# Kernel optimization log

Measured on AMD Instinct MI355X. Metric: run time of the kernel, lower is better.

## Reference

```python
import jax, jax.numpy as jnp
import numpy as np

N_NEURON = 128
N_RULES = 512
BATCH = 4096


def setup_inputs() -> dict:
    key = jax.random.key(0)
    k1, k2, k3, k4, k5 = jax.random.split(key, 5)
    x = jax.random.normal(k1, (N_NEURON, BATCH, N_RULES), dtype=jnp.float32)
    head_w = jax.random.normal(k2, (N_NEURON, N_RULES), dtype=jnp.float32) * (1.0 / np.sqrt(N_RULES))
    head_b = jax.random.normal(k3, (N_NEURON,), dtype=jnp.float32) * 0.01
    foot_w = jax.random.normal(k4, (2, N_NEURON), dtype=jnp.float32) * (1.0 / np.sqrt(N_NEURON))
    foot_b = jax.random.normal(k5, (2,), dtype=jnp.float32) * 0.01
    return {"x": x, "head_w": head_w, "head_b": head_b, "foot_w": foot_w, "foot_b": foot_b}


def reference(x, head_w, head_b, foot_w, foot_b):
    # Fused form of the per-neuron Linear(n_rules, 1) loop:
    # head[b, n] = x[n, b, :] @ head_w[n, :] + head_b[n]
    head = jnp.einsum("nbr,nr->bn", x, head_w) + head_b  # [B, n_neuron]
    logits = head @ foot_w.T + foot_b                      # [B, 2]
    return jax.nn.softmax(logits, axis=-1)
```

## Files before the change

### kernel.cpp

```cpp
#include <hip/hip_runtime.h>

#define BATCH   4096
#define NRULES  512
#define NNEUR   128

typedef float f32x4 __attribute__((ext_vector_type(4)));

__global__ __launch_bounds__(256) void head_kernel(
    const float* __restrict__ x,
    const float* __restrict__ head_w,
    const float* __restrict__ head_b,
    float* __restrict__ head_t)
{
    const int lane = threadIdx.x & 63;
    const int wave = threadIdx.x >> 6;
    const long long wave_g = (long long)blockIdx.x * 4 + wave;
    const long long rid0 = wave_g * 8;
    const int n  = (int)(rid0 >> 12);
    const int b0 = (int)(rid0 & (BATCH - 1));

    const f32x4* w4 = (const f32x4*)(head_w + (size_t)n * NRULES);
    const f32x4 wA = w4[lane];
    const f32x4 wB = w4[64 + lane];

    const float* xrow = x + rid0 * NRULES;
    float acc[8];
#pragma unroll
    for (int j = 0; j < 8; ++j) {
        const f32x4* xr = (const f32x4*)(xrow + (size_t)j * NRULES);
        f32x4 a = __builtin_nontemporal_load(xr + lane);
        f32x4 b = __builtin_nontemporal_load(xr + 64 + lane);
        acc[j] = a[0]*wA[0] + a[1]*wA[1] + a[2]*wA[2] + a[3]*wA[3]
               + b[0]*wB[0] + b[1]*wB[1] + b[2]*wB[2] + b[3]*wB[3];
    }

#pragma unroll
    for (int j = 0; j < 8; ++j) {
#pragma unroll
        for (int off = 32; off > 0; off >>= 1)
            acc[j] += __shfl_xor(acc[j], off, 64);
    }

    if (lane < 8) {
        float v = (lane == 0) ? acc[0]
                : (lane == 1) ? acc[1]
                : (lane == 2) ? acc[2]
                : (lane == 3) ? acc[3]
                : (lane == 4) ? acc[4]
                : (lane == 5) ? acc[5]
                : (lane == 6) ? acc[6]
                              : acc[7];
        v += head_b[n];
        head_t[(size_t)n * BATCH + b0 + lane] = v;
    }
}

__global__ __launch_bounds__(64) void foot_kernel(
    const float* __restrict__ head_t,
    const float* __restrict__ foot_w,
    const float* __restrict__ foot_b,
    float* __restrict__ out)
{
    const int b = blockIdx.x * 64 + threadIdx.x;

    float l0 = foot_b[0];
    float l1 = foot_b[1];
#pragma unroll 16
    for (int n = 0; n < NNEUR; ++n) {
        const float h = head_t[(size_t)n * BATCH + b];
        l0 = fmaf(h, foot_w[n], l0);
        l1 = fmaf(h, foot_w[NNEUR + n], l1);
    }

    const float m  = fmaxf(l0, l1);
    const float e0 = __expf(l0 - m);
    const float e1 = __expf(l1 - m);
    const float inv = 1.0f / (e0 + e1);
    float2 r;
    r.x = e0 * inv;
    r.y = e1 * inv;
    *(float2*)(out + 2 * b) = r;
}

extern "C" void kernel_launch(void* const* d_in, const int* in_sizes, int n_in,
                              void* d_out, int out_size, void* d_ws, size_t ws_size,
                              hipStream_t stream) {
    const float* x      = (const float*)d_in[0];
    const float* head_w = (const float*)d_in[1];
    const float* head_b = (const float*)d_in[2];
    const float* foot_w = (const float*)d_in[3];
    const float* foot_b = (const float*)d_in[4];
    float* out    = (float*)d_out;
    float* head_t = (float*)d_ws;

    const int grid1 = (NNEUR * BATCH) / (8 * 4);
    head_kernel<<<grid1, 256, 0, stream>>>(x, head_w, head_b, head_t);

    foot_kernel<<<BATCH / 64, 64, 0, stream>>>(head_t, foot_w, foot_b, out);
}
```

Before: 1.257 ms.

## Restructure head kernel to 8 rows per wave-pass and split foot reduction

```diff
diff --git a/kernel.cpp b/kernel.cpp
--- a/kernel.cpp
+++ b/kernel.cpp
@@ -13,73 +13,82 @@
     float* __restrict__ head_t)
 {
     const int lane = threadIdx.x & 63;
-    const int wave = threadIdx.x >> 6;
-    const long long wave_g = (long long)blockIdx.x * 4 + wave;
-    const long long rid0 = wave_g * 8;
-    const int n  = (int)(rid0 >> 12);
-    const int b0 = (int)(rid0 & (BATCH - 1));
+    const int wv   = threadIdx.x >> 6;
+    const int i    = lane & 7;
+    const int q    = lane >> 3;
 
-    const f32x4* w4 = (const f32x4*)(head_w + (size_t)n * NRULES);
-    const f32x4 wA = w4[lane];
-    const f32x4 wB = w4[64 + lane];
+    const int wg    = blockIdx.x * 4 + wv;
+    const int n     = wg >> 6;
+    const int bbase = (wg & 63) << 6;
 
-    const float* xrow = x + rid0 * NRULES;
-    float acc[8];
+    const f32x4* wp = (const f32x4*)(head_w + (size_t)n * NRULES);
+    f32x4 w[16];
 #pragma unroll
-    for (int j = 0; j < 8; ++j) {
-        const f32x4* xr = (const f32x4*)(xrow + (size_t)j * NRULES);
-        f32x4 a = __builtin_nontemporal_load(xr + lane);
-        f32x4 b = __builtin_nontemporal_load(xr + 64 + lane);
-        acc[j] = a[0]*wA[0] + a[1]*wA[1] + a[2]*wA[2] + a[3]*wA[3]
-               + b[0]*wB[0] + b[1]*wB[1] + b[2]*wB[2] + b[3]*wB[3];
-    }
+    for (int k = 0; k < 16; ++k) w[k] = wp[i + 8 * k];
 
+    const float hb = head_b[n];
+    float* hrow = head_t + (size_t)n * BATCH;
+
+#pragma unroll 1
+    for (int c = 0; c < 8; ++c) {
+        const int b0 = bbase + c * 8;
+        const f32x4* xp =
+            (const f32x4*)(x + ((size_t)n * BATCH + b0 + q) * NRULES);
+        f32x4 acc = {0.0f, 0.0f, 0.0f, 0.0f};
 #pragma unroll
-    for (int j = 0; j < 8; ++j) {
-#pragma unroll
-        for (int off = 32; off > 0; off >>= 1)
-            acc[j] += __shfl_xor(acc[j], off, 64);
-    }
-
-    if (lane < 8) {
-        float v = (lane == 0) ? acc[0]
-                : (lane == 1) ? acc[1]
-                : (lane == 2) ? acc[2]
-                : (lane == 3) ? acc[3]
-                : (lane == 4) ? acc[4]
-                : (lane == 5) ? acc[5]
-                : (lane == 6) ? acc[6]
-                              : acc[7];
-        v += head_b[n];
-        head_t[(size_t)n * BATCH + b0 + lane] = v;
+        for (int k = 0; k < 16; ++k) {
+            f32x4 v = xp[i + 8 * k];
+            acc += v * w[k];
+        }
+        float s = (acc[0] + acc[1]) + (acc[2] + acc[3]);
+        s += __shfl_xor(s, 1, 64);
+        s += __shfl_xor(s, 2, 64);
+        s += __shfl_xor(s, 4, 64);
+        if (i == 0) hrow[b0 + q] = s + hb;
     }
 }
 
-__global__ __launch_bounds__(64) void foot_kernel(
+__global__ __launch_bounds__(512) void foot_kernel(
     const float* __restrict__ head_t,
     const float* __restrict__ foot_w,
     const float* __restrict__ foot_b,
     float* __restrict__ out)
 {
-    const int b = blockIdx.x * 64 + threadIdx.x;
+    __shared__ float p0[4][128];
+    __shared__ float p1[4][128];
 
-    float l0 = foot_b[0];
-    float l1 = foot_b[1];
-#pragma unroll 16
-    for (int n = 0; n < NNEUR; ++n) {
-        const float h = head_t[(size_t)n * BATCH + b];
+    const int t  = threadIdx.x;
+    const int bl = t & 127;
+    const int qt = t >> 7;
+    const int b0 = blockIdx.x * 128;
+
+    float l0 = 0.0f, l1 = 0.0f;
+    const int n0 = qt * 32;
+#pragma unroll 8
+    for (int k = 0; k < 32; ++k) {
+        const int n = n0 + k;
+        const float h = head_t[(size_t)n * BATCH + b0 + bl];
         l0 = fmaf(h, foot_w[n], l0);
         l1 = fmaf(h, foot_w[NNEUR + n], l1);
     }
+    p0[qt][bl] = l0;
+    p1[qt][bl] = l1;
+    __syncthreads();
 
-    const float m  = fmaxf(l0, l1);
-    const float e0 = __expf(l0 - m);
-    const float e1 = __expf(l1 - m);
-    const float inv = 1.0f / (e0 + e1);
-    float2 r;
-    r.x = e0 * inv;
-    r.y = e1 * inv;
-    *(float2*)(out + 2 * b) = r;
+    if (t < 128) {
+        float a0 = (p0[0][bl] + p0[1][bl]) + (p0[2][bl] + p0[3][bl]);
+        float a1 = (p1[0][bl] + p1[1][bl]) + (p1[2][bl] + p1[3][bl]);
+        a0 += foot_b[0];
+        a1 += foot_b[1];
+        const float m  = fmaxf(a0, a1);
+        const float e0 = __expf(a0 - m);
+        const float e1 = __expf(a1 - m);
+        const float inv = 1.0f / (e0 + e1);
+        float2 r;
+        r.x = e0 * inv;
+        r.y = e1 * inv;
+        *(float2*)(out + 2 * (b0 + bl)) = r;
+    }
 }
 
 extern "C" void kernel_launch(void* const* d_in, const int* in_sizes, int n_in,
@@ -93,8 +102,7 @@
     float* out    = (float*)d_out;
     float* head_t = (float*)d_ws;
 
-    const int grid1 = (NNEUR * BATCH) / (8 * 4);
-    head_kernel<<<grid1, 256, 0, stream>>>(x, head_w, head_b, head_t);
+    head_kernel<<<2048, 256, 0, stream>>>(x, head_w, head_b, head_t);
 
-    foot_kernel<<<BATCH / 64, 64, 0, stream>>>(head_t, foot_w, foot_b, out);
+    foot_kernel<<<32, 512, 0, stream>>>(head_t, foot_w, foot_b, out);
 }
```

After: 1.343 ms. 1.07x slower.
